# Kernel tuning notes

Hardware: AMD Instinct MI355X
Metric: run time of the kernel (lower is better)

## Reference

```python
import jax, jax.numpy as jnp
import numpy as np

B = 16384
WIDE_DIM = 256          # 32 wide features * dim 8
DEEP_DIM = 1024         # 64 deep features * embedding_dim 16
SHARED = [2048, 1024, 512]
DOMAIN = [512, 256]
NUM_DOMAINS = 8


def setup_inputs() -> dict:
    key = jax.random.key(0)
    ks = jax.random.split(key, 20)
    s = 0.01  # embedding_init_var-style small init
    inp = {
        "wide_features": jax.random.normal(ks[0], (B, WIDE_DIM), jnp.float32),
        "deep_features": jax.random.normal(ks[1], (B, DEEP_DIM), jnp.float32),
        "domain_ids": jax.random.randint(ks[2], (B,), 0, NUM_DOMAINS, jnp.int64),
        # shared MLP (weights stored [in, out])
        "W1": jax.random.normal(ks[3], (DEEP_DIM, SHARED[0]), jnp.float32) * s,
        "b1": jnp.zeros((SHARED[0],), jnp.float32),
        "W2": jax.random.normal(ks[4], (SHARED[0], SHARED[1]), jnp.float32) * s,
        "b2": jnp.zeros((SHARED[1],), jnp.float32),
        "W3": jax.random.normal(ks[5], (SHARED[1], SHARED[2]), jnp.float32) * s,
        "b3": jnp.zeros((SHARED[2],), jnp.float32),
        # domain-specific MLP
        "Wd1": jax.random.normal(ks[6], (SHARED[2], DOMAIN[0]), jnp.float32) * s,
        "bd1": jnp.zeros((DOMAIN[0],), jnp.float32),
        "Wd2": jax.random.normal(ks[7], (DOMAIN[0], DOMAIN[1]), jnp.float32) * s,
        "bd2": jnp.zeros((DOMAIN[1],), jnp.float32),
        # per-domain output heads: Linear(DOMAIN[-1], 1) per domain
        "Wh": jax.random.normal(ks[8], (NUM_DOMAINS, DOMAIN[1]), jnp.float32) * s,
        "bh": jnp.zeros((NUM_DOMAINS,), jnp.float32),
    }
    return inp


def reference(wide_features, deep_features, domain_ids,
              W1, b1, W2, b2, W3, b3, Wd1, bd1, Wd2, bd2, Wh, bh):
    # wide part: sum embedding output to a scalar logit per sample [B, 1]
    wide = jnp.sum(wide_features, axis=1, keepdims=True)
    # shared deep MLP
    h = jax.nn.relu(deep_features @ W1 + b1)
    h = jax.nn.relu(h @ W2 + b2)
    shared = jax.nn.relu(h @ W3 + b3)          # [B, 512]
    # domain-specific tower (shared across domains)
    d = jax.nn.relu(shared @ Wd1 + bd1)
    d = jax.nn.relu(d @ Wd2 + bd2)             # [B, 256]
    # per-sample domain head routing: gather head weights, fused dot
    w = Wh[domain_ids]                          # [B, 256]
    head = jnp.sum(d * w, axis=1, keepdims=True) + bh[domain_ids][:, None]  # [B, 1]
    out = jax.nn.sigmoid(wide + head)
    return (out, shared, d)
```

## Files before the change

kernel.cpp:

```cpp
#include <hip/hip_runtime.h>
#include <hip/hip_bf16.h>


typedef __attribute__((ext_vector_type(8))) short short8;
typedef __attribute__((ext_vector_type(4))) float f32x4;

static __device__ __forceinline__ unsigned short f2bf_bits(float x) {
  __hip_bfloat16 h = __float2bfloat16(x);
  return __builtin_bit_cast(unsigned short, h);
}
static __device__ __forceinline__ float bf_bits2f(unsigned short u) {
  __hip_bfloat16 h = __builtin_bit_cast(__hip_bfloat16, u);
  return __bfloat162float(h);
}

static __device__ __forceinline__ void gload16(const void* g, void* l) {
  __builtin_amdgcn_global_load_lds(
      (const __attribute__((address_space(1))) void*)g,
      (__attribute__((address_space(3))) void*)l, 16, 0, 0);
}

static __device__ __forceinline__ unsigned lds_u32(const void* p) {
  return (unsigned)(uintptr_t)(const __attribute__((address_space(3))) void*)p;
}

static __device__ __forceinline__ short8 dsr(unsigned addr) {
  short8 r;
  asm volatile("ds_read_b128 %0, %1" : "=v"(r) : "v"(addr));
  return r;
}

#define MFMA16(a, b, c) __builtin_amdgcn_mfma_f32_16x16x32_bf16((a), (b), (c), 0, 0, 0)

__global__ void transpose_convert(const float* __restrict__ W,
                                  __hip_bfloat16* __restrict__ Wt,
                                  int K, int N) {
  __shared__ float tile[64][65];
  const int k0 = blockIdx.y * 64;
  const int n0 = blockIdx.x * 64;
  const int t  = threadIdx.x;
  const int tn = t & 63;
  const int t4 = t >> 6;
#pragma unroll
  for (int p = 0; p < 16; ++p) {
    int kl = p * 4 + t4;
    tile[kl][tn] = W[(size_t)(k0 + kl) * N + (n0 + tn)];
  }
  __syncthreads();
#pragma unroll
  for (int p = 0; p < 16; ++p) {
    int nl = p * 4 + t4;
    Wt[(size_t)(n0 + nl) * K + (k0 + tn)] = __float2bfloat16(tile[tn][nl]);
  }
}

__global__ void f32_to_bf16(const float* __restrict__ in,
                            unsigned short* __restrict__ out, int n8) {
  int i = blockIdx.x * blockDim.x + threadIdx.x;
  if (i >= n8) return;
  const f32x4* p = (const f32x4*)in + (size_t)i * 2;
  f32x4 a = p[0], b = p[1];
  short8 o;
  o[0] = (short)f2bf_bits(a[0]); o[1] = (short)f2bf_bits(a[1]);
  o[2] = (short)f2bf_bits(a[2]); o[3] = (short)f2bf_bits(a[3]);
  o[4] = (short)f2bf_bits(b[0]); o[5] = (short)f2bf_bits(b[1]);
  o[6] = (short)f2bf_bits(b[2]); o[7] = (short)f2bf_bits(b[3]);
  *(short8*)(out + (size_t)i * 8) = o;
}

__global__ __launch_bounds__(512, 2) void gemm_8p(
    const __hip_bfloat16* __restrict__ A,
    const __hip_bfloat16* __restrict__ Bt,
    const float* __restrict__ bias,
    __hip_bfloat16* __restrict__ Cb,
    float* __restrict__ Cf,
    int N, int K, int nbx) {
  __shared__ char lds[131072];

  const int tid  = threadIdx.x;
  const int lane = tid & 63;
  const int wid  = tid >> 6;
  const int wm   = wid >> 2;
  const int wn   = wid & 3;

  const int nwg = gridDim.x;
  const int cpx = nwg >> 3;
  const int id  = blockIdx.x;
  const int swz = (id & 7) * cpx + (id >> 3);
  const int bm  = (swz / nbx) * 256;
  const int bn  = (swz % nbx) * 256;

  const int ln15 = lane & 15;
  const unsigned cswz = (unsigned)((((lane >> 4) ^ (lane & 7)) << 4));

  const unsigned lbase = lds_u32(lds);
  const unsigned arow0 = lbase + (unsigned)(wm * 128 + ln15) * 128u + cswz;
  const unsigned brow0 = lbase + 32768u + (unsigned)(wn * 64 + ln15) * 128u + cswz;

  const int nt = K >> 6;

  auto stage = [&](int kt, int half, int isB) {
    const __hip_bfloat16* G = isB ? Bt : A;
    const int blk0 = isB ? bn : bm;
    char* base = lds + ((kt & 1) * 65536) + (isB ? 32768 : 0) + half * 16384;
#pragma unroll
    for (int q = 0; q < 2; ++q) {
      int rl  = half * 128 + q * 64 + (tid >> 3);
      int swc = (tid & 7) ^ ((tid >> 3) & 7);
      gload16(G + (size_t)(blk0 + rl) * K + kt * 64 + swc * 8,
              base + q * 8192 + wid * 1024);
    }
  };

  f32x4 acc[8][4] = {};

  stage(0, 0, 1); stage(0, 0, 0); stage(0, 1, 1); stage(0, 1, 0);
  if (nt > 1) {
    stage(1, 0, 1); stage(1, 0, 0);
    asm volatile("s_waitcnt vmcnt(4)");
  } else {
    asm volatile("s_waitcnt vmcnt(0)");
  }
  __builtin_amdgcn_s_barrier();

  for (int t = 0; t < nt; ++t) {
    const unsigned po = (unsigned)(t & 1) * 65536u;
    short8 a_[4][2], b0_[2][2], b1_[2][2];

#pragma unroll
    for (int mi = 0; mi < 4; ++mi) {
      unsigned ad = arow0 + po + (unsigned)(mi * 2048);
      a_[mi][0] = dsr(ad); a_[mi][1] = dsr(ad ^ 64u);
    }
#pragma unroll
    for (int nj = 0; nj < 2; ++nj) {
      unsigned bd = brow0 + po + (unsigned)(nj * 2048);
      b0_[nj][0] = dsr(bd); b0_[nj][1] = dsr(bd ^ 64u);
    }
    if (t + 1 < nt) stage(t + 1, 1, 1);
    asm volatile("s_waitcnt lgkmcnt(8)");
    __builtin_amdgcn_s_barrier();
    asm volatile("s_waitcnt lgkmcnt(0)");
    __builtin_amdgcn_sched_barrier(0);
    __builtin_amdgcn_s_setprio(1);
#pragma unroll
    for (int mi = 0; mi < 4; ++mi)
#pragma unroll
      for (int nj = 0; nj < 2; ++nj)
#pragma unroll
        for (int kk = 0; kk < 2; ++kk)
          acc[mi][nj] = MFMA16(a_[mi][kk], b0_[nj][kk], acc[mi][nj]);
    __builtin_amdgcn_s_setprio(0);
    __builtin_amdgcn_s_barrier();

#pragma unroll
    for (int nj = 0; nj < 2; ++nj) {
      unsigned bd = brow0 + po + (unsigned)((nj + 2) * 2048);
      b1_[nj][0] = dsr(bd); b1_[nj][1] = dsr(bd ^ 64u);
    }
    if (t + 1 < nt) stage(t + 1, 1, 0);
    __builtin_amdgcn_s_barrier();
    asm volatile("s_waitcnt lgkmcnt(0)");
    __builtin_amdgcn_sched_barrier(0);
    __builtin_amdgcn_s_setprio(1);
#pragma unroll
    for (int mi = 0; mi < 4; ++mi)
#pragma unroll
      for (int nj = 0; nj < 2; ++nj)
#pragma unroll
        for (int kk = 0; kk < 2; ++kk)
          acc[mi][nj + 2] = MFMA16(a_[mi][kk], b1_[nj][kk], acc[mi][nj + 2]);
    __builtin_amdgcn_s_setprio(0);
    __builtin_amdgcn_s_barrier();

#pragma unroll
    for (int mi = 0; mi < 4; ++mi) {
      unsigned ad = arow0 + po + (unsigned)((mi + 4) * 2048);
      a_[mi][0] = dsr(ad); a_[mi][1] = dsr(ad ^ 64u);
    }
    if (t + 2 < nt) stage(t + 2, 0, 1);
    __builtin_amdgcn_s_barrier();
    asm volatile("s_waitcnt lgkmcnt(0)");
    __builtin_amdgcn_sched_barrier(0);
    __builtin_amdgcn_s_setprio(1);
#pragma unroll
    for (int mi = 0; mi < 4; ++mi)
#pragma unroll
      for (int nj = 0; nj < 2; ++nj)
#pragma unroll
        for (int kk = 0; kk < 2; ++kk)
          acc[mi + 4][nj] = MFMA16(a_[mi][kk], b0_[nj][kk], acc[mi + 4][nj]);
    __builtin_amdgcn_s_setprio(0);
    __builtin_amdgcn_s_barrier();

    if (t + 2 < nt) stage(t + 2, 0, 0);
    __builtin_amdgcn_s_barrier();
    __builtin_amdgcn_s_setprio(1);
#pragma unroll
    for (int mi = 0; mi < 4; ++mi)
#pragma unroll
      for (int nj = 0; nj < 2; ++nj)
#pragma unroll
        for (int kk = 0; kk < 2; ++kk)
          acc[mi + 4][nj + 2] = MFMA16(a_[mi][kk], b1_[nj][kk], acc[mi + 4][nj + 2]);
    __builtin_amdgcn_s_setprio(0);
    if (t + 2 < nt) asm volatile("s_waitcnt vmcnt(4)");
    else            asm volatile("s_waitcnt vmcnt(0)");
    __builtin_amdgcn_s_barrier();
  }

  float biasv[4];
#pragma unroll
  for (int nj = 0; nj < 4; ++nj)
    biasv[nj] = bias[bn + wn * 64 + nj * 16 + ln15];

#pragma unroll
  for (int mi = 0; mi < 8; ++mi) {
    int row0 = bm + wm * 128 + mi * 16 + (lane >> 4) * 4;
#pragma unroll
    for (int nj = 0; nj < 4; ++nj) {
      int col = bn + wn * 64 + nj * 16 + ln15;
#pragma unroll
      for (int r = 0; r < 4; ++r) {
        float v = acc[mi][nj][r] + biasv[nj];
        v = v > 0.f ? v : 0.f;
        size_t idx = (size_t)(row0 + r) * N + col;
        Cb[idx] = __float2bfloat16(v);
        if (Cf) Cf[idx] = v;
      }
    }
  }
}

__global__ __launch_bounds__(256, 2) void gemm_bt(
    const __hip_bfloat16* __restrict__ A,
    const __hip_bfloat16* __restrict__ Bt,
    const float* __restrict__ bias,
    __hip_bfloat16* __restrict__ Cb,
    float* __restrict__ Cf,
    int N, int K) {
  __shared__ char lds[32768];

  const int tid  = threadIdx.x;
  const int lane = tid & 63;
  const int wid  = tid >> 6;
  const int wm   = wid >> 1;
  const int wn   = wid & 1;
  const int bm   = blockIdx.y * 128;
  const int bn   = blockIdx.x * 128;

  f32x4 acc[4][4] = {};

  const int srow = tid >> 3;
  const int sk   = (tid & 7) * 8;
  const int kTiles = K >> 6;

  for (int kt = 0; kt < kTiles; ++kt) {
    __syncthreads();
    const __hip_bfloat16* ga = A  + (size_t)(bm + srow) * K + kt * 64 + sk;
    const __hip_bfloat16* gb = Bt + (size_t)(bn + srow) * K + kt * 64 + sk;
#pragma unroll
    for (int p = 0; p < 4; ++p) {
      gload16(ga + (size_t)(p * 32) * K, &lds[p * 4096 + wid * 1024]);
      gload16(gb + (size_t)(p * 32) * K, &lds[16384 + p * 4096 + wid * 1024]);
    }
    __syncthreads();

#pragma unroll
    for (int kk = 0; kk < 2; ++kk) {
      short8 avec[4], bvec[4];
#pragma unroll
      for (int i = 0; i < 4; ++i) {
        int row = wm * 64 + i * 16 + (lane & 15);
        avec[i] = *(const short8*)&lds[row * 128 + kk * 64 + (lane >> 4) * 16];
      }
#pragma unroll
      for (int j = 0; j < 4; ++j) {
        int row = wn * 64 + j * 16 + (lane & 15);
        bvec[j] = *(const short8*)&lds[16384 + row * 128 + kk * 64 + (lane >> 4) * 16];
      }
#pragma unroll
      for (int i = 0; i < 4; ++i)
#pragma unroll
        for (int j = 0; j < 4; ++j)
          acc[i][j] = MFMA16(avec[i], bvec[j], acc[i][j]);
    }
  }

  float biasv[4];
#pragma unroll
  for (int j = 0; j < 4; ++j)
    biasv[j] = bias[bn + wn * 64 + j * 16 + (lane & 15)];

#pragma unroll
  for (int i = 0; i < 4; ++i) {
    int row0 = bm + wm * 64 + i * 16 + (lane >> 4) * 4;
#pragma unroll
    for (int j = 0; j < 4; ++j) {
      int col = bn + wn * 64 + j * 16 + (lane & 15);
#pragma unroll
      for (int r = 0; r < 4; ++r) {
        float v = acc[i][j][r] + biasv[j];
        v = v > 0.f ? v : 0.f;
        size_t idx = (size_t)(row0 + r) * N + col;
        Cb[idx] = __float2bfloat16(v);
        if (Cf) Cf[idx] = v;
      }
    }
  }
}

__global__ __launch_bounds__(256) void head_kernel(
    const float* __restrict__ wide,
    const __hip_bfloat16* __restrict__ D,
    const int* __restrict__ dom,
    const float* __restrict__ Wh,
    const float* __restrict__ bh,
    float* __restrict__ out, int B) {
  const int wid  = threadIdx.x >> 6;
  const int lane = threadIdx.x & 63;
  const int row  = blockIdx.x * 4 + wid;
  if (row >= B) return;
  const int dm = dom[row];

  f32x4 wv = ((const f32x4*)(wide + (size_t)row * 256))[lane];
  float tot = wv[0] + wv[1] + wv[2] + wv[3];

  const unsigned short* drow = (const unsigned short*)(D + (size_t)row * 256);
  ushort4 dv = ((const ushort4*)drow)[lane];
  f32x4 hv = ((const f32x4*)(Wh + (size_t)dm * 256))[lane];
  tot += bf_bits2f(dv.x) * hv[0] + bf_bits2f(dv.y) * hv[1] +
         bf_bits2f(dv.z) * hv[2] + bf_bits2f(dv.w) * hv[3];

#pragma unroll
  for (int off = 32; off > 0; off >>= 1) tot += __shfl_xor(tot, off);

  if (lane == 0) {
    float x = tot + bh[dm];
    out[row] = 1.f / (1.f + __expf(-x));
  }
}

extern "C" void kernel_launch(void* const* d_in, const int* in_sizes, int n_in,
                              void* d_out, int out_size, void* d_ws, size_t ws_size,
                              hipStream_t stream) {
  const float* wide = (const float*)d_in[0];
  const float* deep = (const float*)d_in[1];
  const int*   dom  = (const int*)d_in[2];
  const float* W1  = (const float*)d_in[3];
  const float* b1  = (const float*)d_in[4];
  const float* W2  = (const float*)d_in[5];
  const float* b2  = (const float*)d_in[6];
  const float* W3  = (const float*)d_in[7];
  const float* b3  = (const float*)d_in[8];
  const float* Wd1 = (const float*)d_in[9];
  const float* bd1 = (const float*)d_in[10];
  const float* Wd2 = (const float*)d_in[11];
  const float* bd2 = (const float*)d_in[12];
  const float* Wh  = (const float*)d_in[13];
  const float* bh  = (const float*)d_in[14];
  float* out = (float*)d_out;

  const int B = 16384;
  char* ws = (char*)d_ws;
  __hip_bfloat16* buf0 = (__hip_bfloat16*)ws;
  __hip_bfloat16* buf1 = (__hip_bfloat16*)(ws + 33554432ull);
  __hip_bfloat16* W1t  = (__hip_bfloat16*)(ws + 100663296ull);
  __hip_bfloat16* W2t  = W1t + 2048 * 1024;
  __hip_bfloat16* W3t  = W2t + 1024 * 2048;
  __hip_bfloat16* Wd1t = W3t + 512 * 1024;
  __hip_bfloat16* Wd2t = Wd1t + 512 * 512;

  transpose_convert<<<dim3(2048 / 64, 1024 / 64), 256, 0, stream>>>(W1, W1t, 1024, 2048);
  transpose_convert<<<dim3(1024 / 64, 2048 / 64), 256, 0, stream>>>(W2, W2t, 2048, 1024);
  transpose_convert<<<dim3(512 / 64, 1024 / 64), 256, 0, stream>>>(W3, W3t, 1024, 512);
  transpose_convert<<<dim3(512 / 64, 512 / 64), 256, 0, stream>>>(Wd1, Wd1t, 512, 512);
  transpose_convert<<<dim3(256 / 64, 512 / 64), 256, 0, stream>>>(Wd2, Wd2t, 512, 256);

  {
    int n8 = B * 1024 / 8;
    f32_to_bf16<<<(n8 + 255) / 256, 256, 0, stream>>>(deep, (unsigned short*)buf0, n8);
  }

  float* shared_out = out + B;
  float* d_out_f    = out + B + (size_t)B * 512;

  gemm_8p<<<dim3((2048 / 256) * (B / 256)), 512, 0, stream>>>(
      buf0, W1t, b1, buf1, nullptr, 2048, 1024, 2048 / 256);
  gemm_8p<<<dim3((1024 / 256) * (B / 256)), 512, 0, stream>>>(
      buf1, W2t, b2, buf0, nullptr, 1024, 2048, 1024 / 256);
  gemm_bt<<<dim3(512 / 128, B / 128), 256, 0, stream>>>(buf0, W3t, b3, buf1, shared_out, 512, 1024);
  gemm_bt<<<dim3(512 / 128, B / 128), 256, 0, stream>>>(buf1, Wd1t, bd1, buf0, nullptr, 512, 512);
  gemm_bt<<<dim3(256 / 128, B / 128), 256, 0, stream>>>(buf0, Wd2t, bd2, buf1, d_out_f, 256, 512);

  head_kernel<<<B / 4, 256, 0, stream>>>(wide, buf1, dom, Wh, bh, out, B);
}
```

Measured before the change: 240.5 us.

## Restructure GEMM main loop barriers and split LDS reads for MFMA overlap

```diff
diff --git a/kernel.cpp b/kernel.cpp
--- a/kernel.cpp
+++ b/kernel.cpp
@@ -99,59 +99,58 @@
 
   const int nt = K >> 6;
 
+  const int swc = (tid & 7) ^ ((tid >> 3) & 7);
+  const __hip_bfloat16* baseA = A  + (size_t)(bm + (tid >> 3)) * K + swc * 8;
+  const __hip_bfloat16* baseB = Bt + (size_t)(bn + (tid >> 3)) * K + swc * 8;
+  const unsigned ldst0 = (unsigned)(wid * 1024);
+
   auto stage = [&](int kt, int half, int isB) {
-    const __hip_bfloat16* G = isB ? Bt : A;
-    const int blk0 = isB ? bn : bm;
-    char* base = lds + ((kt & 1) * 65536) + (isB ? 32768 : 0) + half * 16384;
+    const __hip_bfloat16* base = isB ? baseB : baseA;
+    char* dst = lds + ((kt & 1) * 65536) + (isB ? 32768 : 0) + half * 16384;
 #pragma unroll
     for (int q = 0; q < 2; ++q) {
-      int rl  = half * 128 + q * 64 + (tid >> 3);
-      int swc = (tid & 7) ^ ((tid >> 3) & 7);
-      gload16(G + (size_t)(blk0 + rl) * K + kt * 64 + swc * 8,
-              base + q * 8192 + wid * 1024);
+      gload16(base + (size_t)((half * 128 + q * 64) * K + kt * 64),
+              dst + q * 8192 + ldst0);
     }
   };
 
   f32x4 acc[8][4] = {};
 
   stage(0, 0, 1); stage(0, 0, 0); stage(0, 1, 1); stage(0, 1, 0);
-  if (nt > 1) {
-    stage(1, 0, 1); stage(1, 0, 0);
-    asm volatile("s_waitcnt vmcnt(4)");
-  } else {
-    asm volatile("s_waitcnt vmcnt(0)");
-  }
-  __builtin_amdgcn_s_barrier();
+  if (nt > 1) { stage(1, 0, 1); stage(1, 0, 0); }
 
   for (int t = 0; t < nt; ++t) {
     const unsigned po = (unsigned)(t & 1) * 65536u;
     short8 a_[4][2], b0_[2][2], b1_[2][2];
 
-#pragma unroll
-    for (int mi = 0; mi < 4; ++mi) {
-      unsigned ad = arow0 + po + (unsigned)(mi * 2048);
-      a_[mi][0] = dsr(ad); a_[mi][1] = dsr(ad ^ 64u);
-    }
-#pragma unroll
-    for (int nj = 0; nj < 2; ++nj) {
-      unsigned bd = brow0 + po + (unsigned)(nj * 2048);
-      b0_[nj][0] = dsr(bd); b0_[nj][1] = dsr(bd ^ 64u);
-    }
+    if (t + 1 < nt) asm volatile("s_waitcnt vmcnt(4)");
+    else            asm volatile("s_waitcnt vmcnt(0)");
+    __builtin_amdgcn_s_barrier();
+#pragma unroll
+    for (int mi = 0; mi < 4; ++mi) a_[mi][0] = dsr(arow0 + po + (unsigned)(mi * 2048));
+#pragma unroll
+    for (int nj = 0; nj < 2; ++nj) b0_[nj][0] = dsr(brow0 + po + (unsigned)(nj * 2048));
+#pragma unroll
+    for (int mi = 0; mi < 4; ++mi) a_[mi][1] = dsr((arow0 + po + (unsigned)(mi * 2048)) ^ 64u);
+#pragma unroll
+    for (int nj = 0; nj < 2; ++nj) b0_[nj][1] = dsr((brow0 + po + (unsigned)(nj * 2048)) ^ 64u);
     if (t + 1 < nt) stage(t + 1, 1, 1);
-    asm volatile("s_waitcnt lgkmcnt(8)");
-    __builtin_amdgcn_s_barrier();
+    asm volatile("s_waitcnt lgkmcnt(6)");
+    __builtin_amdgcn_sched_barrier(0);
+    __builtin_amdgcn_s_setprio(1);
+#pragma unroll
+    for (int mi = 0; mi < 4; ++mi)
+#pragma unroll
+      for (int nj = 0; nj < 2; ++nj)
+        acc[mi][nj] = MFMA16(a_[mi][0], b0_[nj][0], acc[mi][nj]);
     asm volatile("s_waitcnt lgkmcnt(0)");
     __builtin_amdgcn_sched_barrier(0);
-    __builtin_amdgcn_s_setprio(1);
 #pragma unroll
     for (int mi = 0; mi < 4; ++mi)
 #pragma unroll
       for (int nj = 0; nj < 2; ++nj)
-#pragma unroll
-        for (int kk = 0; kk < 2; ++kk)
-          acc[mi][nj] = MFMA16(a_[mi][kk], b0_[nj][kk], acc[mi][nj]);
+        acc[mi][nj] = MFMA16(a_[mi][1], b0_[nj][1], acc[mi][nj]);
     __builtin_amdgcn_s_setprio(0);
-    __builtin_amdgcn_s_barrier();
 
 #pragma unroll
     for (int nj = 0; nj < 2; ++nj) {
@@ -164,49 +163,44 @@
     __builtin_amdgcn_sched_barrier(0);
     __builtin_amdgcn_s_setprio(1);
 #pragma unroll
-    for (int mi = 0; mi < 4; ++mi)
-#pragma unroll
-      for (int nj = 0; nj < 2; ++nj)
-#pragma unroll
-        for (int kk = 0; kk < 2; ++kk)
+    for (int kk = 0; kk < 2; ++kk)
+#pragma unroll
+      for (int mi = 0; mi < 4; ++mi)
+#pragma unroll
+        for (int nj = 0; nj < 2; ++nj)
           acc[mi][nj + 2] = MFMA16(a_[mi][kk], b1_[nj][kk], acc[mi][nj + 2]);
     __builtin_amdgcn_s_setprio(0);
-    __builtin_amdgcn_s_barrier();
 
 #pragma unroll
     for (int mi = 0; mi < 4; ++mi) {
       unsigned ad = arow0 + po + (unsigned)((mi + 4) * 2048);
       a_[mi][0] = dsr(ad); a_[mi][1] = dsr(ad ^ 64u);
     }
+    __builtin_amdgcn_s_barrier();
     if (t + 2 < nt) stage(t + 2, 0, 1);
-    __builtin_amdgcn_s_barrier();
     asm volatile("s_waitcnt lgkmcnt(0)");
     __builtin_amdgcn_sched_barrier(0);
     __builtin_amdgcn_s_setprio(1);
 #pragma unroll
-    for (int mi = 0; mi < 4; ++mi)
-#pragma unroll
-      for (int nj = 0; nj < 2; ++nj)
-#pragma unroll
-        for (int kk = 0; kk < 2; ++kk)
+    for (int kk = 0; kk < 2; ++kk)
+#pragma unroll
+      for (int mi = 0; mi < 4; ++mi)
+#pragma unroll
+        for (int nj = 0; nj < 2; ++nj)
           acc[mi + 4][nj] = MFMA16(a_[mi][kk], b0_[nj][kk], acc[mi + 4][nj]);
     __builtin_amdgcn_s_setprio(0);
+
     __builtin_amdgcn_s_barrier();
-
     if (t + 2 < nt) stage(t + 2, 0, 0);
-    __builtin_amdgcn_s_barrier();
     __builtin_amdgcn_s_setprio(1);
 #pragma unroll
-    for (int mi = 0; mi < 4; ++mi)
-#pragma unroll
-      for (int nj = 0; nj < 2; ++nj)
-#pragma unroll
-        for (int kk = 0; kk < 2; ++kk)
+    for (int kk = 0; kk < 2; ++kk)
+#pragma unroll
+      for (int mi = 0; mi < 4; ++mi)
+#pragma unroll
+        for (int nj = 0; nj < 2; ++nj)
           acc[mi + 4][nj + 2] = MFMA16(a_[mi][kk], b1_[nj][kk], acc[mi + 4][nj + 2]);
     __builtin_amdgcn_s_setprio(0);
-    if (t + 2 < nt) asm volatile("s_waitcnt vmcnt(4)");
-    else            asm volatile("s_waitcnt vmcnt(0)");
-    __builtin_amdgcn_s_barrier();
   }
 
   float biasv[4];
```

New measurement: 234.2 us. -2.6%, faster.
